# Kernel tuning notes

Measured on AMD Instinct MI355X. Metric: run time of the kernel, lower is better.

Reference implementation:

```python
import jax, jax.numpy as jnp
import numpy as np

N_NODES = 100000
NEG_SLOPE = 0.2  # PyG GATConv default


def gat_conv(x, src, dst, W, a_src, a_dst, bias, heads, out_c, concat):
    """PyG-style GATConv (eval mode, no dropout). src->dst message flow,
    softmax over incoming edges of dst. Self-loops assumed already added."""
    N = x.shape[0]
    h = (x @ W).reshape(N, heads, out_c)              # [N,H,C]
    alpha_s = (h * a_src[None]).sum(-1)               # [N,H]
    alpha_d = (h * a_dst[None]).sum(-1)               # [N,H]
    e = jax.nn.leaky_relu(alpha_s[src] + alpha_d[dst], NEG_SLOPE)  # [E,H]
    m = jax.ops.segment_max(e, dst, num_segments=N)   # segment softmax (stable)
    e = jnp.exp(e - m[dst])
    denom = jax.ops.segment_sum(e, dst, num_segments=N)
    alpha = e / (denom[dst] + 1e-16)                  # [E,H]
    msg = h[src] * alpha[:, :, None]                  # [E,H,C]
    out = jax.ops.segment_sum(msg, dst, num_segments=N)  # [N,H,C]
    out = out.reshape(N, heads * out_c) if concat else out.mean(axis=1)
    return out + bias


def _forward(x, edge_index, query_edges, W1, as1, ad1, b1, W2, as2, ad2, b2):
    N = x.shape[0]
    # add self loops (PyG GATConv default add_self_loops=True)
    loop = jnp.arange(N, dtype=edge_index.dtype)
    src = jnp.concatenate([edge_index[0], loop])
    dst = jnp.concatenate([edge_index[1], loop])
    h = gat_conv(x, src, dst, W1, as1, ad1, b1, heads=8, out_c=8, concat=True)
    h = jax.nn.elu(h)
    z = gat_conv(h, src, dst, W2, as2, ad2, b2, heads=1, out_c=64, concat=False)
    # dot-product decode on query edges
    raw = (z[query_edges[0]] * z[query_edges[1]]).sum(-1)
    return jax.nn.sigmoid(raw)


def setup_inputs() -> dict:
    key = jax.random.key(0)
    ks = jax.random.split(key, 12)
    N, D, H1, C1, HID = N_NODES, 128, 8, 8, 64
    E, Q = 1600000, 100000
    x = jax.random.normal(ks[0], (N, D), dtype=jnp.float32)
    edge_index = jax.random.randint(ks[1], (2, E), 0, N, dtype=jnp.int64)
    query_edges = jax.random.randint(ks[2], (2, Q), 0, N, dtype=jnp.int64)
    s1 = 1.0 / np.sqrt(D)
    s2 = 1.0 / np.sqrt(HID)
    return {
        "x": x,
        "edge_index": edge_index,
        "query_edges": query_edges,
        "W1": jax.random.normal(ks[3], (D, H1 * C1), dtype=jnp.float32) * s1,
        "as1": jax.random.normal(ks[4], (H1, C1), dtype=jnp.float32) * s1,
        "ad1": jax.random.normal(ks[5], (H1, C1), dtype=jnp.float32) * s1,
        "b1": jnp.zeros((H1 * C1,), dtype=jnp.float32),
        "W2": jax.random.normal(ks[6], (HID, HID), dtype=jnp.float32) * s2,
        "as2": jax.random.normal(ks[7], (1, HID), dtype=jnp.float32) * s2,
        "ad2": jax.random.normal(ks[8], (1, HID), dtype=jnp.float32) * s2,
        "b2": jnp.zeros((HID,), dtype=jnp.float32),
    }


def reference(x, edge_index, query_edges, W1, as1, ad1, b1, W2, as2, ad2, b2):
    return _forward(x, edge_index, query_edges, W1, as1, ad1, b1, W2, as2, ad2, b2)
```

## Files before the change

kernel.cpp:

```cpp
#include <hip/hip_runtime.h>
#include <math.h>

constexpr float NEG_SLOPE = 0.2f;

__device__ __forceinline__ float lrelu(float x) { return x > 0.f ? x : NEG_SLOPE * x; }

__device__ __forceinline__ int readlane_i(int v, int l) {
    return __builtin_amdgcn_readlane(v, l);
}
__device__ __forceinline__ float readlane_f(float v, int l) {
    return __uint_as_float(__builtin_amdgcn_readlane(__float_as_uint(v), l));
}
__device__ __forceinline__ unsigned short f2b(float f) {
    unsigned u = __float_as_uint(f);
    unsigned r = u + 0x7FFFu + ((u >> 16) & 1u);
    return (unsigned short)(r >> 16);
}
__device__ __forceinline__ float b2f(unsigned short s) {
    return __uint_as_float((unsigned)s << 16);
}

#define MAC16(av, bv) \
    acc[0][0] += av.x*bv.x; acc[0][1] += av.x*bv.y; acc[0][2] += av.x*bv.z; acc[0][3] += av.x*bv.w; \
    acc[1][0] += av.y*bv.x; acc[1][1] += av.y*bv.y; acc[1][2] += av.y*bv.z; acc[1][3] += av.y*bv.w; \
    acc[2][0] += av.z*bv.x; acc[2][1] += av.z*bv.y; acc[2][2] += av.z*bv.z; acc[2][3] += av.z*bv.w; \
    acc[3][0] += av.w*bv.x; acc[3][1] += av.w*bv.y; acc[3][2] += av.w*bv.z; acc[3][3] += av.w*bv.w;

__global__ __launch_bounds__(256) void gemm1_kernel(
    const float* __restrict__ X, const float* __restrict__ W,
    const float* __restrict__ a_s, const float* __restrict__ a_d,
    unsigned short* __restrict__ Hb, unsigned short* __restrict__ as1b,
    float* __restrict__ adn, int N)
{
    __shared__ float At[128 * 64];
    __shared__ float Bs[128 * 64];
    const int tid = threadIdx.x;
    const int r_base = blockIdx.x * 64;
    {
        const float4* W4 = (const float4*)W;
        float4* B4 = (float4*)Bs;
#pragma unroll
        for (int it = 0; it < 8; ++it) B4[tid + it * 256] = W4[tid + it * 256];
    }
    {
        const float4* X4 = (const float4*)X;
#pragma unroll
        for (int it = 0; it < 2; ++it) {
            int t = tid + it * 256;
            int rg = t & 15, cg = t >> 4;
            float4 rw[4];
#pragma unroll
            for (int j = 0; j < 4; ++j) {
                int r = r_base + rg * 4 + j;
                rw[j] = (r < N) ? X4[(size_t)r * 32 + cg] : make_float4(0.f, 0.f, 0.f, 0.f);
            }
            int rsw = 4 * (rg ^ (cg & 15));
            int k0 = cg * 4;
            *(float4*)&At[(k0    ) * 64 + rsw] = make_float4(rw[0].x, rw[1].x, rw[2].x, rw[3].x);
            *(float4*)&At[(k0 + 1) * 64 + rsw] = make_float4(rw[0].y, rw[1].y, rw[2].y, rw[3].y);
            *(float4*)&At[(k0 + 2) * 64 + rsw] = make_float4(rw[0].z, rw[1].z, rw[2].z, rw[3].z);
            *(float4*)&At[(k0 + 3) * 64 + rsw] = make_float4(rw[0].w, rw[1].w, rw[2].w, rw[3].w);
        }
    }
    __syncthreads();
    const int m  = tid & 15;
    const int ci = (tid >> 4) * 4;
    float acc[4][4] = {};
#pragma unroll 4
    for (int kq = 0; kq < 32; ++kq) {
        int aoff = kq * 256 + 4 * (m ^ (kq & 15));
        int boff = kq * 256 + ci;
        float4 a0 = *(const float4*)&At[aoff];
        float4 a1 = *(const float4*)&At[aoff + 64];
        float4 a2 = *(const float4*)&At[aoff + 128];
        float4 a3 = *(const float4*)&At[aoff + 192];
        float4 b0 = *(const float4*)&Bs[boff];
        float4 b1 = *(const float4*)&Bs[boff + 64];
        float4 b2 = *(const float4*)&Bs[boff + 128];
        float4 b3 = *(const float4*)&Bs[boff + 192];
        MAC16(a0, b0); MAC16(a1, b1); MAC16(a2, b2); MAC16(a3, b3);
    }
    float asv[4] = {a_s[ci], a_s[ci + 1], a_s[ci + 2], a_s[ci + 3]};
    float adv[4] = {a_d[ci], a_d[ci + 1], a_d[ci + 2], a_d[ci + 3]};
    int head = ci >> 3;
    bool owner = ((tid >> 4) & 1) == 0;
#pragma unroll
    for (int j = 0; j < 4; ++j) {
        int r = r_base + m * 4 + j;
        if (r < N) {
            ushort4 pk;
            pk.x = f2b(acc[j][0]); pk.y = f2b(acc[j][1]);
            pk.z = f2b(acc[j][2]); pk.w = f2b(acc[j][3]);
            *(ushort4*)&Hb[(size_t)r * 64 + ci] = pk;
        }
        float ps = acc[j][0]*asv[0] + acc[j][1]*asv[1] + acc[j][2]*asv[2] + acc[j][3]*asv[3];
        float pd = acc[j][0]*adv[0] + acc[j][1]*adv[1] + acc[j][2]*adv[2] + acc[j][3]*adv[3];
        ps += __shfl_xor(ps, 16);
        pd += __shfl_xor(pd, 16);
        if (owner && r < N) { as1b[r * 8 + head] = f2b(ps); adn[r * 8 + head] = pd; }
    }
}

__global__ __launch_bounds__(256) void gemm2_kernel(
    const float* __restrict__ X, const float* __restrict__ W,
    const float* __restrict__ a_s, const float* __restrict__ a_d,
    unsigned short* __restrict__ Zb, unsigned short* __restrict__ as2b,
    float* __restrict__ adn, int N)
{
    __shared__ float At[64 * 64];
    __shared__ float Bs[64 * 64];
    __shared__ float Ps[4][16][4], Pd[4][16][4];
    const int tid = threadIdx.x;
    const int r_base = blockIdx.x * 64;
    {
        const float4* W4 = (const float4*)W;
        float4* B4 = (float4*)Bs;
#pragma unroll
        for (int it = 0; it < 4; ++it) B4[tid + it * 256] = W4[tid + it * 256];
    }
    {
        const float4* X4 = (const float4*)X;
        int rg = tid & 15, cg = tid >> 4;
        float4 rw[4];
#pragma unroll
        for (int j = 0; j < 4; ++j) {
            int r = r_base + rg * 4 + j;
            rw[j] = (r < N) ? X4[(size_t)r * 16 + cg] : make_float4(0.f, 0.f, 0.f, 0.f);
        }
        int rsw = 4 * (rg ^ (cg & 15));
        int k0 = cg * 4;
        *(float4*)&At[(k0    ) * 64 + rsw] = make_float4(rw[0].x, rw[1].x, rw[2].x, rw[3].x);
        *(float4*)&At[(k0 + 1) * 64 + rsw] = make_float4(rw[0].y, rw[1].y, rw[2].y, rw[3].y);
        *(float4*)&At[(k0 + 2) * 64 + rsw] = make_float4(rw[0].z, rw[1].z, rw[2].z, rw[3].z);
        *(float4*)&At[(k0 + 3) * 64 + rsw] = make_float4(rw[0].w, rw[1].w, rw[2].w, rw[3].w);
    }
    __syncthreads();
    const int m  = tid & 15;
    const int ci = (tid >> 4) * 4;
    float acc[4][4] = {};
#pragma unroll 4
    for (int kq = 0; kq < 16; ++kq) {
        int aoff = kq * 256 + 4 * (m ^ (kq & 15));
        int boff = kq * 256 + ci;
        float4 a0 = *(const float4*)&At[aoff];
        float4 a1 = *(const float4*)&At[aoff + 64];
        float4 a2 = *(const float4*)&At[aoff + 128];
        float4 a3 = *(const float4*)&At[aoff + 192];
        float4 b0 = *(const float4*)&Bs[boff];
        float4 b1 = *(const float4*)&Bs[boff + 64];
        float4 b2 = *(const float4*)&Bs[boff + 128];
        float4 b3 = *(const float4*)&Bs[boff + 192];
        MAC16(a0, b0); MAC16(a1, b1); MAC16(a2, b2); MAC16(a3, b3);
    }
    float asv[4] = {a_s[ci], a_s[ci + 1], a_s[ci + 2], a_s[ci + 3]};
    float adv[4] = {a_d[ci], a_d[ci + 1], a_d[ci + 2], a_d[ci + 3]};
    int w = tid >> 6;
    float ps[4], pd[4];
#pragma unroll
    for (int j = 0; j < 4; ++j) {
        int r = r_base + m * 4 + j;
        if (r < N) {
            ushort4 pk;
            pk.x = f2b(acc[j][0]); pk.y = f2b(acc[j][1]);
            pk.z = f2b(acc[j][2]); pk.w = f2b(acc[j][3]);
            *(ushort4*)&Zb[(size_t)r * 64 + ci] = pk;
        }
        ps[j] = acc[j][0]*asv[0] + acc[j][1]*asv[1] + acc[j][2]*asv[2] + acc[j][3]*asv[3];
        pd[j] = acc[j][0]*adv[0] + acc[j][1]*adv[1] + acc[j][2]*adv[2] + acc[j][3]*adv[3];
        ps[j] += __shfl_xor(ps[j], 16); ps[j] += __shfl_xor(ps[j], 32);
        pd[j] += __shfl_xor(pd[j], 16); pd[j] += __shfl_xor(pd[j], 32);
    }
    if (((tid >> 4) & 3) == 0) {
#pragma unroll
        for (int j = 0; j < 4; ++j) { Ps[w][m][j] = ps[j]; Pd[w][m][j] = pd[j]; }
    }
    __syncthreads();
    if (tid < 64) {
        int r = r_base + tid;
        if (r < N) {
            int mm = tid >> 2, jj = tid & 3;
            as2b[r] = f2b(Ps[0][mm][jj] + Ps[1][mm][jj] + Ps[2][mm][jj] + Ps[3][mm][jj]);
            adn[r]  = Pd[0][mm][jj] + Pd[1][mm][jj] + Pd[2][mm][jj] + Pd[3][mm][jj];
        }
    }
}

__global__ __launch_bounds__(256) void bhist_kernel(
    const int* __restrict__ dst, int E, int T, int shift, int NB, int NT,
    int* __restrict__ thist)
{
    __shared__ int h[256];
    int t = blockIdx.x, tid = threadIdx.x;
    for (int i = tid; i < NB; i += 256) h[i] = 0;
    __syncthreads();
    int e0 = t * T, e1 = min(E, e0 + T);
    for (int e = e0 + tid; e < e1; e += 256) atomicAdd(&h[dst[e] >> shift], 1);
    __syncthreads();
    for (int i = tid; i < NB; i += 256) thist[(size_t)i * NT + t] = h[i];
}

__global__ __launch_bounds__(256) void btot_kernel(
    const int* __restrict__ thist, int NT, int* __restrict__ btot)
{
    int b = blockIdx.x, tid = threadIdx.x;
    __shared__ int wsum[4];
    int s = 0;
    for (int t = tid; t < NT; t += 256) s += thist[(size_t)b * NT + t];
#pragma unroll
    for (int d = 1; d < 64; d <<= 1) s += __shfl_xor(s, d);
    if ((tid & 63) == 0) wsum[tid >> 6] = s;
    __syncthreads();
    if (tid == 0) btot[b] = wsum[0] + wsum[1] + wsum[2] + wsum[3];
}

__global__ __launch_bounds__(64) void bbase_kernel(
    const int* __restrict__ btot, int NB, int* __restrict__ bbase)
{
    int lane = threadIdx.x;
    int carry = 0;
    for (int base = 0; base < NB; base += 64) {
        int i = base + lane;
        int v = (i < NB) ? btot[i] : 0;
        int incl = v;
#pragma unroll
        for (int d = 1; d < 64; d <<= 1) {
            int t = __shfl_up(incl, d);
            if (lane >= d) incl += t;
        }
        if (i < NB) bbase[i] = carry + incl - v;
        carry += __shfl(incl, 63);
    }
    if (lane == 0) bbase[NB] = carry;
}

__global__ __launch_bounds__(256) void bofs_kernel(
    int* __restrict__ thist, int NT, const int* __restrict__ bbase)
{
    int b = blockIdx.x, tid = threadIdx.x;
    int lane = tid & 63, w = tid >> 6;
    __shared__ int wsum[4];
    __shared__ int carry_s;
    if (tid == 0) carry_s = bbase[b];
    __syncthreads();
    for (int base = 0; base < NT; base += 256) {
        int t = base + tid;
        int v = (t < NT) ? thist[(size_t)b * NT + t] : 0;
        int incl = v;
#pragma unroll
        for (int d = 1; d < 64; d <<= 1) {
            int x = __shfl_up(incl, d);
            if (lane >= d) incl += x;
        }
        if (lane == 63) wsum[w] = incl;
        __syncthreads();
        int woff = 0;
        for (int i = 0; i < w; ++i) woff += wsum[i];
        if (t < NT) thist[(size_t)b * NT + t] = carry_s + woff + incl - v;
        __syncthreads();
        if (tid == 0) carry_s += wsum[0] + wsum[1] + wsum[2] + wsum[3];
        __syncthreads();
    }
}

__global__ __launch_bounds__(256) void bscatter_kernel(
    const int* __restrict__ src, const int* __restrict__ dst, int E, int T,
    int shift, int NB, int NT, const int* __restrict__ thist, int2* __restrict__ stg)
{
    __shared__ int cur[256];
    int t = blockIdx.x, tid = threadIdx.x;
    for (int i = tid; i < NB; i += 256) cur[i] = thist[(size_t)i * NT + t];
    __syncthreads();
    int e0 = t * T, e1 = min(E, e0 + T);
    for (int e = e0 + tid; e < e1; e += 256) {
        int d = dst[e];
        int pos = atomicAdd(&cur[d >> shift], 1);
        stg[pos] = make_int2(src[e], d);
    }
}

__global__ __launch_bounds__(256) void bbuild_kernel(
    const int2* __restrict__ stg, const int* __restrict__ bbase, int shift, int N,
    int* __restrict__ offv, int* __restrict__ cnt, int* __restrict__ csr)
{
    __shared__ int lcnt[1024], loff[1024], lfill[1024];
    int b = blockIdx.x, tid = threadIdx.x;
    int bs = 1 << shift;
    int n0 = b << shift;
    int e0 = bbase[b], e1 = bbase[b + 1];
    for (int i = tid; i < bs; i += 256) lcnt[i] = 0;
    __syncthreads();
    for (int e = e0 + tid; e < e1; e += 256) atomicAdd(&lcnt[stg[e].y - n0], 1);
    __syncthreads();
    if (tid < 64) {
        int seg = bs >> 6;
        int j0 = tid * seg;
        int local = 0;
        for (int j = 0; j < seg; ++j) {
            int n = n0 + j0 + j;
            local += (n < N) ? lcnt[j0 + j] + 1 : 0;
        }
        int incl = local;
#pragma unroll
        for (int d = 1; d < 64; d <<= 1) {
            int t2 = __shfl_up(incl, d);
            if (tid >= d) incl += t2;
        }
        int run = incl - local;
        for (int j = 0; j < seg; ++j) {
            int n = n0 + j0 + j;
            int v = (n < N) ? lcnt[j0 + j] + 1 : 0;
            loff[j0 + j] = run;
            run += v;
        }
    }
    __syncthreads();
    int csr_base = e0 + n0;
    for (int i = tid; i < bs; i += 256) {
        int n = n0 + i;
        if (n < N) {
            int o = csr_base + loff[i];
            offv[n] = o;
            cnt[n] = lcnt[i];
            csr[o] = n;
            lfill[i] = loff[i] + 1;
        }
    }
    __syncthreads();
    for (int e = e0 + tid; e < e1; e += 256) {
        int2 p = stg[e];
        int pos = atomicAdd(&lfill[p.y - n0], 1);
        csr[csr_base + pos] = p.x;
    }
}

__global__ __launch_bounds__(256) void gat1_kernel(
    const unsigned short* __restrict__ Hb, const unsigned short* __restrict__ as1b,
    const float* __restrict__ adn, const float* __restrict__ b1,
    const int* __restrict__ offv, const int* __restrict__ cnt,
    const int* __restrict__ csr, float* __restrict__ h2, int N)
{
    int n = blockIdx.x * 4 + (threadIdx.x >> 6);
    if (n >= N) return;
    int lane = threadIdx.x & 63;
    int base = offv[n];
    int deg = cnt[n] + 1;
    int hh = lane >> 3;
    int jC = lane >> 3, hC = lane & 7;
    float adC = adn[n * 8 + hC];
    float acc = 0.f, psum = 0.f;

    if (deg <= 64) {
        int sreg = csr[base + (lane < deg ? lane : 0)];
        int c0 = 0;
        for (; c0 + 8 <= deg; c0 += 8) {
            int sj = __shfl(sreg, c0 + jC);
            float p = __expf(lrelu(b2f(as1b[sj * 8 + hC]) + adC));
#pragma unroll
            for (int jj = 0; jj < 8; ++jj) {
                float pj = __shfl(p, jj * 8 + hh);
                int s = readlane_i(sreg, c0 + jj);
                acc += pj * b2f(Hb[(size_t)s * 64 + lane]);
                psum += pj;
            }
        }
        if (c0 < deg) {
            int idx = c0 + jC;
            int sj = __shfl(sreg, idx);
            float p = (idx < deg) ? __expf(lrelu(b2f(as1b[sj * 8 + hC]) + adC)) : 0.f;
            int rem = deg - c0;
            for (int jj = 0; jj < rem; ++jj) {
                float pj = __shfl(p, jj * 8 + hh);
                int s = readlane_i(sreg, c0 + jj);
                acc += pj * b2f(Hb[(size_t)s * 64 + lane]);
                psum += pj;
            }
        }
    } else {
        float ad = adn[n * 8 + hh];
        for (int k = 0; k < deg; ++k) {
            int s = __builtin_amdgcn_readfirstlane(csr[base + k]);
            float p = __expf(lrelu(b2f(as1b[s * 8 + hh]) + ad));
            acc += p * b2f(Hb[(size_t)s * 64 + lane]);
            psum += p;
        }
    }
    float v = acc / psum + b1[lane];
    h2[(size_t)n * 64 + lane] = v > 0.f ? v : __expf(v) - 1.f;
}

__global__ __launch_bounds__(256) void gat2_kernel(
    const unsigned short* __restrict__ Zb, const unsigned short* __restrict__ as2b,
    const float* __restrict__ adn, const float* __restrict__ b2,
    const int* __restrict__ offv, const int* __restrict__ cnt,
    const int* __restrict__ csr, float* __restrict__ out, int N)
{
    int n = blockIdx.x * 4 + (threadIdx.x >> 6);
    if (n >= N) return;
    int lane = threadIdx.x & 63;
    int base = offv[n];
    int deg = cnt[n] + 1;
    float ad = adn[n];
    float acc = 0.f, psum;

    if (deg <= 64) {
        int sreg = csr[base + (lane < deg ? lane : 0)];
        float aE = b2f(as2b[sreg]);
        float p = (lane < deg) ? __expf(lrelu(aE + ad)) : 0.f;
        psum = p;
#pragma unroll
        for (int d = 1; d < 64; d <<= 1) psum += __shfl_xor(psum, d);
        int k = 0;
        for (; k + 4 <= deg; k += 4) {
            int s0 = readlane_i(sreg, k), s1 = readlane_i(sreg, k + 1),
                s2 = readlane_i(sreg, k + 2), s3 = readlane_i(sreg, k + 3);
            float p0 = readlane_f(p, k), p1 = readlane_f(p, k + 1),
                  p2 = readlane_f(p, k + 2), p3 = readlane_f(p, k + 3);
            acc += p0 * b2f(Zb[(size_t)s0 * 64 + lane]);
            acc += p1 * b2f(Zb[(size_t)s1 * 64 + lane]);
            acc += p2 * b2f(Zb[(size_t)s2 * 64 + lane]);
            acc += p3 * b2f(Zb[(size_t)s3 * 64 + lane]);
        }
        for (; k < deg; ++k)
            acc += readlane_f(p, k) * b2f(Zb[(size_t)readlane_i(sreg, k) * 64 + lane]);
    } else {
        psum = 0.f;
        for (int k = 0; k < deg; ++k) {
            int s = __builtin_amdgcn_readfirstlane(csr[base + k]);
            float p = __expf(lrelu(b2f(as2b[s]) + ad));
            acc += p * b2f(Zb[(size_t)s * 64 + lane]);
            psum += p;
        }
    }
    out[(size_t)n * 64 + lane] = acc / psum + b2[lane];
}

__global__ __launch_bounds__(256) void decode_kernel(
    const float* __restrict__ z2, const int* __restrict__ q, int Q, float* __restrict__ out)
{
    int i = blockIdx.x * 4 + (threadIdx.x >> 6);
    if (i >= Q) return;
    int lane = threadIdx.x & 63;
    int a = q[i], b = q[Q + i];
    float v = z2[(size_t)a * 64 + lane] * z2[(size_t)b * 64 + lane];
#pragma unroll
    for (int d = 1; d < 64; d <<= 1) v += __shfl_xor(v, d);
    if (lane == 0) out[i] = 1.f / (1.f + __expf(-v));
}

extern "C" void kernel_launch(void* const* d_in, const int* in_sizes, int n_in,
                              void* d_out, int out_size, void* d_ws, size_t ws_size,
                              hipStream_t stream)
{
    const float* x   = (const float*)d_in[0];
    const int*   ei  = (const int*)d_in[1];
    const int*   qe  = (const int*)d_in[2];
    const float* W1  = (const float*)d_in[3];
    const float* as1 = (const float*)d_in[4];
    const float* ad1 = (const float*)d_in[5];
    const float* b1  = (const float*)d_in[6];
    const float* W2  = (const float*)d_in[7];
    const float* as2 = (const float*)d_in[8];
    const float* ad2 = (const float*)d_in[9];
    const float* b2  = (const float*)d_in[10];

    const int N = in_sizes[0] / 128;
    const int E = in_sizes[1] / 2;
    const int Q = in_sizes[2] / 2;

    float* out = (float*)d_out;

    int shift = 9;
    while ((((N + (1 << shift) - 1) >> shift)) > 256 && shift < 10) shift++;
    const int NB = (N + (1 << shift) - 1) >> shift;
    const int T  = 4096;
    const int NT = (E + T - 1) / T;

    char* ws = (char*)d_ws;
    size_t o = 0;
    auto alloc = [&](size_t bytes) -> void* {
        void* p = ws + o;
        o += (bytes + 255) & ~(size_t)255;
        return p;
    };
    unsigned short* hb   = (unsigned short*)alloc((size_t)N * 64 * 2);
    float* f32buf        = (float*)alloc((size_t)N * 64 * 4);
    unsigned short* as1b = (unsigned short*)alloc((size_t)N * 8 * 2);
    float* adn1          = (float*)alloc((size_t)N * 8 * 4);
    unsigned short* as2b = (unsigned short*)alloc((size_t)N * 2);
    float* adn2          = (float*)alloc((size_t)N * 4);
    int*   cnt    = (int*)alloc((size_t)N * 4);
    int*   offv   = (int*)alloc((size_t)N * 4);
    int*   csr    = (int*)alloc((size_t)(E + N) * 4);
    int*   thist  = (int*)alloc((size_t)NB * NT * 4);
    int*   btot   = (int*)alloc((size_t)NB * 4);
    int*   bbase  = (int*)alloc((size_t)(NB + 1) * 4);
    int2*  stg    = (int2*)alloc((size_t)E * 8);

    const int* esrc = ei;
    const int* edst = ei + E;

    int nodeBlocks4 = (N + 3) / 4;
    int tileBlocks  = (N + 63) / 64;

    gemm1_kernel<<<tileBlocks, 256, 0, stream>>>(x, W1, as1, ad1, hb, as1b, adn1, N);
    bhist_kernel<<<NT, 256, 0, stream>>>(edst, E, T, shift, NB, NT, thist);
    btot_kernel<<<NB, 256, 0, stream>>>(thist, NT, btot);
    bbase_kernel<<<1, 64, 0, stream>>>(btot, NB, bbase);
    bofs_kernel<<<NB, 256, 0, stream>>>(thist, NT, bbase);
    bscatter_kernel<<<NT, 256, 0, stream>>>(esrc, edst, E, T, shift, NB, NT, thist, stg);
    bbuild_kernel<<<NB, 256, 0, stream>>>(stg, bbase, shift, N, offv, cnt, csr);
    gat1_kernel<<<nodeBlocks4, 256, 0, stream>>>(hb, as1b, adn1, b1, offv, cnt, csr, f32buf, N);
    gemm2_kernel<<<tileBlocks, 256, 0, stream>>>(f32buf, W2, as2, ad2, hb, as2b, adn2, N);
    gat2_kernel<<<nodeBlocks4, 256, 0, stream>>>(hb, as2b, adn2, b2, offv, cnt, csr, f32buf, N);
    decode_kernel<<<(Q + 3) / 4, 256, 0, stream>>>(f32buf, qe, Q, out);
}
```

Baseline: 350.7 us.

## Vectorize neighbor gathers: 16 lanes per row, 4 edges per wave in parallel

In gat1 and gat2 each wave now splits into four 16-lane groups. Each group loads a whole 64-channel bf16 row with one 8-byte load per lane, so four neighbor rows are in flight per iteration instead of one row read with 2-byte loads. The partial sums are combined across groups with xor-shuffles, and 16 lanes write the result as float4. The decode kernel likewise handles four query pairs per wave with float4 loads. This raises memory-level parallelism and access width at the cost of extra shuffles and fewer lanes active at the end.

```diff
diff --git a/kernel.cpp b/kernel.cpp
--- a/kernel.cpp
+++ b/kernel.cpp
@@ -7,9 +7,6 @@
 
 __device__ __forceinline__ int readlane_i(int v, int l) {
     return __builtin_amdgcn_readlane(v, l);
-}
-__device__ __forceinline__ float readlane_f(float v, int l) {
-    return __uint_as_float(__builtin_amdgcn_readlane(__float_as_uint(v), l));
 }
 __device__ __forceinline__ unsigned short f2b(float f) {
     unsigned u = __float_as_uint(f);
@@ -344,48 +341,63 @@
     int lane = threadIdx.x & 63;
     int base = offv[n];
     int deg = cnt[n] + 1;
-    int hh = lane >> 3;
-    int jC = lane >> 3, hC = lane & 7;
-    float adC = adn[n * 8 + hC];
-    float acc = 0.f, psum = 0.f;
 
     if (deg <= 64) {
+        int cg   = lane >> 4;
+        int ch4  = (lane & 15) * 4;
+        int headA = (lane & 15) >> 1;
+        int jC = lane >> 3, hC = lane & 7;
+        float adC = adn[n * 8 + hC];
         int sreg = csr[base + (lane < deg ? lane : 0)];
-        int c0 = 0;
-        for (; c0 + 8 <= deg; c0 += 8) {
-            int sj = __shfl(sreg, c0 + jC);
-            float p = __expf(lrelu(b2f(as1b[sj * 8 + hC]) + adC));
-#pragma unroll
-            for (int jj = 0; jj < 8; ++jj) {
-                float pj = __shfl(p, jj * 8 + hh);
-                int s = readlane_i(sreg, c0 + jj);
-                acc += pj * b2f(Hb[(size_t)s * 64 + lane]);
+        float a0 = 0.f, a1 = 0.f, a2 = 0.f, a3 = 0.f, psum = 0.f;
+        int nch = (deg + 7) >> 3;
+        for (int c = 0; c < nch; ++c) {
+            int c0 = c * 8;
+            int idxC = c0 + jC;
+            int sj = __shfl(sreg, idxC);
+            float p = (idxC < deg) ? __expf(lrelu(b2f(as1b[sj * 8 + hC]) + adC)) : 0.f;
+#pragma unroll
+            for (int sub = 0; sub < 2; ++sub) {
+                int el = sub * 4 + cg;
+                int s  = __shfl(sreg, c0 + el);
+                float pj = __shfl(p, el * 8 + headA);
+                uint2 d = *(const uint2*)(Hb + (size_t)s * 64 + ch4);
+                a0 += pj * __uint_as_float(d.x << 16);
+                a1 += pj * __uint_as_float(d.x & 0xffff0000u);
+                a2 += pj * __uint_as_float(d.y << 16);
+                a3 += pj * __uint_as_float(d.y & 0xffff0000u);
                 psum += pj;
             }
         }
-        if (c0 < deg) {
-            int idx = c0 + jC;
-            int sj = __shfl(sreg, idx);
-            float p = (idx < deg) ? __expf(lrelu(b2f(as1b[sj * 8 + hC]) + adC)) : 0.f;
-            int rem = deg - c0;
-            for (int jj = 0; jj < rem; ++jj) {
-                float pj = __shfl(p, jj * 8 + hh);
-                int s = readlane_i(sreg, c0 + jj);
-                acc += pj * b2f(Hb[(size_t)s * 64 + lane]);
-                psum += pj;
-            }
+        a0 += __shfl_xor(a0, 16); a0 += __shfl_xor(a0, 32);
+        a1 += __shfl_xor(a1, 16); a1 += __shfl_xor(a1, 32);
+        a2 += __shfl_xor(a2, 16); a2 += __shfl_xor(a2, 32);
+        a3 += __shfl_xor(a3, 16); a3 += __shfl_xor(a3, 32);
+        psum += __shfl_xor(psum, 16); psum += __shfl_xor(psum, 32);
+        if (lane < 16) {
+            float rp = 1.f / psum;
+            float4 bb = *(const float4*)&b1[ch4];
+            float v0 = a0 * rp + bb.x, v1 = a1 * rp + bb.y,
+                  v2 = a2 * rp + bb.z, v3 = a3 * rp + bb.w;
+            v0 = v0 > 0.f ? v0 : __expf(v0) - 1.f;
+            v1 = v1 > 0.f ? v1 : __expf(v1) - 1.f;
+            v2 = v2 > 0.f ? v2 : __expf(v2) - 1.f;
+            v3 = v3 > 0.f ? v3 : __expf(v3) - 1.f;
+            *(float4*)&h2[(size_t)n * 64 + ch4] = make_float4(v0, v1, v2, v3);
         }
     } else {
+        int hh = lane >> 3;
         float ad = adn[n * 8 + hh];
+        float acc = 0.f, psum = 0.f;
         for (int k = 0; k < deg; ++k) {
             int s = __builtin_amdgcn_readfirstlane(csr[base + k]);
             float p = __expf(lrelu(b2f(as1b[s * 8 + hh]) + ad));
             acc += p * b2f(Hb[(size_t)s * 64 + lane]);
             psum += p;
         }
-    }
-    float v = acc / psum + b1[lane];
-    h2[(size_t)n * 64 + lane] = v > 0.f ? v : __expf(v) - 1.f;
+        float v = acc / psum + b1[lane];
+        h2[(size_t)n * 64 + lane] = v > 0.f ? v : __expf(v) - 1.f;
+    }
 }
 
 __global__ __launch_bounds__(256) void gat2_kernel(
@@ -400,51 +412,64 @@
     int base = offv[n];
     int deg = cnt[n] + 1;
     float ad = adn[n];
-    float acc = 0.f, psum;
 
     if (deg <= 64) {
+        int cg  = lane >> 4;
+        int ch4 = (lane & 15) * 4;
         int sreg = csr[base + (lane < deg ? lane : 0)];
-        float aE = b2f(as2b[sreg]);
-        float p = (lane < deg) ? __expf(lrelu(aE + ad)) : 0.f;
-        psum = p;
+        float p = (lane < deg) ? __expf(lrelu(b2f(as2b[sreg]) + ad)) : 0.f;
+        float psum = p;
 #pragma unroll
         for (int d = 1; d < 64; d <<= 1) psum += __shfl_xor(psum, d);
-        int k = 0;
-        for (; k + 4 <= deg; k += 4) {
-            int s0 = readlane_i(sreg, k), s1 = readlane_i(sreg, k + 1),
-                s2 = readlane_i(sreg, k + 2), s3 = readlane_i(sreg, k + 3);
-            float p0 = readlane_f(p, k), p1 = readlane_f(p, k + 1),
-                  p2 = readlane_f(p, k + 2), p3 = readlane_f(p, k + 3);
-            acc += p0 * b2f(Zb[(size_t)s0 * 64 + lane]);
-            acc += p1 * b2f(Zb[(size_t)s1 * 64 + lane]);
-            acc += p2 * b2f(Zb[(size_t)s2 * 64 + lane]);
-            acc += p3 * b2f(Zb[(size_t)s3 * 64 + lane]);
-        }
-        for (; k < deg; ++k)
-            acc += readlane_f(p, k) * b2f(Zb[(size_t)readlane_i(sreg, k) * 64 + lane]);
+        float a0 = 0.f, a1 = 0.f, a2 = 0.f, a3 = 0.f;
+        int nkk = (deg + 3) >> 2;
+        for (int kk = 0; kk < nkk; ++kk) {
+            int idx = kk * 4 + cg;
+            int s = __shfl(sreg, idx);
+            float pj = __shfl(p, idx);
+            uint2 d = *(const uint2*)(Zb + (size_t)s * 64 + ch4);
+            a0 += pj * __uint_as_float(d.x << 16);
+            a1 += pj * __uint_as_float(d.x & 0xffff0000u);
+            a2 += pj * __uint_as_float(d.y << 16);
+            a3 += pj * __uint_as_float(d.y & 0xffff0000u);
+        }
+        a0 += __shfl_xor(a0, 16); a0 += __shfl_xor(a0, 32);
+        a1 += __shfl_xor(a1, 16); a1 += __shfl_xor(a1, 32);
+        a2 += __shfl_xor(a2, 16); a2 += __shfl_xor(a2, 32);
+        a3 += __shfl_xor(a3, 16); a3 += __shfl_xor(a3, 32);
+        if (lane < 16) {
+            float rp = 1.f / psum;
+            float4 bb = *(const float4*)&b2[ch4];
+            *(float4*)&out[(size_t)n * 64 + ch4] =
+                make_float4(a0 * rp + bb.x, a1 * rp + bb.y, a2 * rp + bb.z, a3 * rp + bb.w);
+        }
     } else {
-        psum = 0.f;
+        float acc = 0.f, psum = 0.f;
         for (int k = 0; k < deg; ++k) {
             int s = __builtin_amdgcn_readfirstlane(csr[base + k]);
             float p = __expf(lrelu(b2f(as2b[s]) + ad));
             acc += p * b2f(Zb[(size_t)s * 64 + lane]);
             psum += p;
         }
-    }
-    out[(size_t)n * 64 + lane] = acc / psum + b2[lane];
+        out[(size_t)n * 64 + lane] = acc / psum + b2[lane];
+    }
 }
 
 __global__ __launch_bounds__(256) void decode_kernel(
     const float* __restrict__ z2, const int* __restrict__ q, int Q, float* __restrict__ out)
 {
-    int i = blockIdx.x * 4 + (threadIdx.x >> 6);
-    if (i >= Q) return;
+    int w = blockIdx.x * 4 + (threadIdx.x >> 6);
     int lane = threadIdx.x & 63;
-    int a = q[i], b = q[Q + i];
-    float v = z2[(size_t)a * 64 + lane] * z2[(size_t)b * 64 + lane];
-#pragma unroll
-    for (int d = 1; d < 64; d <<= 1) v += __shfl_xor(v, d);
-    if (lane == 0) out[i] = 1.f / (1.f + __expf(-v));
+    int cg = lane >> 4, ch4 = (lane & 15) * 4;
+    int i = w * 4 + cg;
+    int ic = min(i, Q - 1);
+    int a = q[ic], b = q[Q + ic];
+    float4 va = *(const float4*)&z2[(size_t)a * 64 + ch4];
+    float4 vb = *(const float4*)&z2[(size_t)b * 64 + ch4];
+    float v = va.x * vb.x + va.y * vb.y + va.z * vb.z + va.w * vb.w;
+    v += __shfl_xor(v, 1); v += __shfl_xor(v, 2);
+    v += __shfl_xor(v, 4); v += __shfl_xor(v, 8);
+    if ((lane & 15) == 0 && i < Q) out[i] = 1.f / (1.f + __expf(-v));
 }
 
 extern "C" void kernel_launch(void* const* d_in, const int* in_sizes, int n_in,
@@ -512,5 +537,5 @@
     gat1_kernel<<<nodeBlocks4, 256, 0, stream>>>(hb, as1b, adn1, b1, offv, cnt, csr, f32buf, N);
     gemm2_kernel<<<tileBlocks, 256, 0, stream>>>(f32buf, W2, as2, ad2, hb, as2b, adn2, N);
     gat2_kernel<<<nodeBlocks4, 256, 0, stream>>>(hb, as2b, adn2, b2, offv, cnt, csr, f32buf, N);
-    decode_kernel<<<(Q + 3) / 4, 256, 0, stream>>>(f32buf, qe, Q, out);
-}
+    decode_kernel<<<(Q + 15) / 16, 256, 0, stream>>>(f32buf, qe, Q, out);
+}
```

New measurement: 330.3 us. -5.8%, faster.
